# Kernel optimization log

Measured on AMD Instinct MI355X. Metric: run time of the kernel, lower is better.

## Reference

```python
import jax, jax.numpy as jnp
import numpy as np

D_MODEL = 1024
N_HEADS = 16
D_HEAD = D_MODEL // N_HEADS


def setup_inputs() -> dict:
    key = jax.random.key(0)
    ks = jax.random.split(key, 11)
    B, T = 2, 2048
    s = 1.0 / np.sqrt(D_MODEL)
    return {
        "query": jax.random.normal(ks[0], (B, T, D_MODEL), dtype=jnp.float32),
        "key": jax.random.normal(ks[1], (B, T, D_MODEL), dtype=jnp.float32),
        "value": jax.random.normal(ks[2], (B, T, D_MODEL), dtype=jnp.float32),
        "Wq": jax.random.normal(ks[3], (D_MODEL, D_MODEL), dtype=jnp.float32) * s,
        "bq": jnp.zeros((D_MODEL,), dtype=jnp.float32),
        "Wk": jax.random.normal(ks[4], (D_MODEL, D_MODEL), dtype=jnp.float32) * s,
        "bk": jnp.zeros((D_MODEL,), dtype=jnp.float32),
        "Wv": jax.random.normal(ks[5], (D_MODEL, D_MODEL), dtype=jnp.float32) * s,
        "bv": jnp.zeros((D_MODEL,), dtype=jnp.float32),
        "Wh": jax.random.normal(ks[6], (D_MODEL, D_MODEL), dtype=jnp.float32) * s,
        "bh": jnp.zeros((D_MODEL,), dtype=jnp.float32),
    }


def reference(query, key, value, Wq, bq, Wk, bk, Wv, bv, Wh, bh):
    B, T_src, _ = query.shape
    T_dst = key.shape[1]
    # torch nn.Linear: y = x @ W.T + b
    Q = query @ Wq.T + bq          # (B, T_src, D)
    K = key @ Wk.T + bk            # (B, T_dst, D)
    V = value @ Wv.T + bv          # (B, T_dst, D)
    Q = Q.reshape(B, T_src, N_HEADS, D_HEAD).transpose(0, 2, 1, 3)  # (B,H,Ts,dh)
    K = K.reshape(B, T_dst, N_HEADS, D_HEAD).transpose(0, 2, 1, 3)  # (B,H,Td,dh)
    V = V.reshape(B, T_dst, N_HEADS, D_HEAD).transpose(0, 2, 1, 3)  # (B,H,Td,dh)
    dot = jnp.einsum("bhsd,bhtd->bhst", Q, K) / np.sqrt(D_HEAD)     # (B,H,Ts,Td)
    scores = jax.nn.softmax(dot, axis=-1)
    out = jnp.einsum("bhst,bhtd->bhsd", scores, V)  # (B,H,Ts,dh)
    # Faithful to source: reshape WITHOUT transposing heads back (source quirk)
    out = out.reshape(B, T_src, D_MODEL)
    return out @ Wh.T + bh
```

## Files before the change

kernel.cpp:

```cpp
#include <hip/hip_runtime.h>
#include <hip/hip_bf16.h>
#include <stdint.h>

typedef __attribute__((ext_vector_type(8))) short bf16x8;
typedef __attribute__((ext_vector_type(4))) short bf16x4;
typedef __attribute__((ext_vector_type(4))) float f32x4;
typedef __attribute__((ext_vector_type(16))) float f32x16;
typedef __attribute__((ext_vector_type(4))) unsigned int u32x4;
typedef __attribute__((ext_vector_type(2))) __bf16 bf16x2n;

#define DEVI __device__ __forceinline__

DEVI short f2b(float f) {
  union { float f; uint32_t u; } x; x.f = f;
  uint32_t r = x.u + 0x7fffu + ((x.u >> 16) & 1u);
  return (short)(r >> 16);
}

DEVI unsigned packbf(float a, float b) {
  bf16x2n v; v[0] = (__bf16)a; v[1] = (__bf16)b;
  return __builtin_bit_cast(unsigned, v);
}

DEVI float exp2f_(float x) {
#if __has_builtin(__builtin_amdgcn_exp2f)
  return __builtin_amdgcn_exp2f(x);
#else
  return __expf(x * 0.6931471805599453f);
#endif
}

DEVI void plswap(unsigned& a, unsigned& b) {
#if __has_builtin(__builtin_amdgcn_permlane32_swap)
  auto r = __builtin_amdgcn_permlane32_swap(a, b, false, false);
  a = r[0]; b = r[1];
#else
  asm volatile("s_nop 1\n\tv_permlane32_swap_b32 %0, %1\n\ts_nop 1" : "+v"(a), "+v"(b));
#endif
}

DEVI float xmax32(float x) {
  unsigned a = __builtin_bit_cast(unsigned, x), b = a;
  plswap(a, b);
  return fmaxf(__builtin_bit_cast(float, a), __builtin_bit_cast(float, b));
}
DEVI float xsum32(float x) {
  unsigned a = __builtin_bit_cast(unsigned, x), b = a;
  plswap(a, b);
  return __builtin_bit_cast(float, a) + __builtin_bit_cast(float, b);
}

DEVI void async16(const void* gsrc, void* lds) {
  __builtin_amdgcn_global_load_lds((__attribute__((address_space(1))) void*)gsrc,
                                   (__attribute__((address_space(3))) void*)lds,
                                   16, 0, 0);
}

__global__ __launch_bounds__(256) void cvt_all(const float* __restrict__ q,
                                               const float* __restrict__ k,
                                               const float* __restrict__ v,
                                               const float* __restrict__ wq,
                                               const float* __restrict__ wk,
                                               const float* __restrict__ wv,
                                               const float* __restrict__ wh,
                                               short* __restrict__ ws) {
  const size_t MT = 4096ull * 1024ull;
  int bid = blockIdx.x;
  const float* src; short* dst; int idx;
  if (bid < 6144) {
    int r = bid >> 11;
    src = (r == 0) ? q : (r == 1) ? k : v;
    dst = ws + (size_t)r * MT;
    idx = (bid & 2047) * 256 + threadIdx.x;
  } else {
    int r = (bid - 6144) >> 9;
    src = (r == 0) ? wq : (r == 1) ? wk : (r == 2) ? wv : wh;
    dst = ws + 3 * MT + (size_t)r * (1024 * 1024);
    idx = ((bid - 6144) & 511) * 256 + threadIdx.x;
  }
  f32x4 a = ((const f32x4*)src)[2 * idx];
  f32x4 b = ((const f32x4*)src)[2 * idx + 1];
  bf16x8 o;
  o[0]=f2b(a[0]); o[1]=f2b(a[1]); o[2]=f2b(a[2]); o[3]=f2b(a[3]);
  o[4]=f2b(b[0]); o[5]=f2b(b[1]); o[6]=f2b(b[2]); o[7]=f2b(b[3]);
  ((bf16x8*)dst)[idx] = o;
}

__global__ __launch_bounds__(256) void gemm_qkv(const short* __restrict__ A0,
                                                const short* __restrict__ A1,
                                                const short* __restrict__ A2,
                                                const short* __restrict__ W0,
                                                const short* __restrict__ W1,
                                                const short* __restrict__ W2,
                                                const float* __restrict__ b0,
                                                const float* __restrict__ b1,
                                                const float* __restrict__ b2,
                                                short* __restrict__ O0,
                                                short* __restrict__ O1,
                                                short* __restrict__ O2) {
  constexpr int Kd = 1024, Nd = 1024;
  const int z = blockIdx.z;
  const short* A  = (z == 0) ? A0 : (z == 1) ? A1 : A2;
  const short* Bt = (z == 0) ? W0 : (z == 1) ? W1 : W2;
  const float* bias = (z == 0) ? b0 : (z == 1) ? b1 : b2;

  __shared__ __attribute__((aligned(128))) char smem[32768];
  char* As = smem;
  char* Bs = smem + 16384;
  const int tid = threadIdx.x, lane = tid & 63, wave = tid >> 6;
  const int m0 = blockIdx.x * 128, n0 = blockIdx.y * 128;
  const int wr = wave >> 1, wc = wave & 1;

  f32x4 acc[4][4];
#pragma unroll
  for (int i = 0; i < 4; i++)
#pragma unroll
    for (int j = 0; j < 4; j++) acc[i][j] = (f32x4)0.0f;

  for (int k0 = 0; k0 < Kd; k0 += 64) {
#pragma unroll
    for (int it = 0; it < 4; ++it) {
      int ci = it * 256 + tid;
      int r = ci >> 3, c8 = ci & 7;
      int sc = c8 ^ (r & 7);
      async16((const char*)A + ((size_t)(m0 + r) * Kd + k0) * 2 + sc * 16,
              As + it * 4096 + wave * 1024);
      async16((const char*)Bt + ((size_t)(n0 + r) * Kd + k0) * 2 + sc * 16,
              Bs + it * 4096 + wave * 1024);
    }
    __syncthreads();
#pragma unroll
    for (int kk = 0; kk < 2; ++kk) {
      bf16x8 af[4], bf[4];
#pragma unroll
      for (int i = 0; i < 4; i++) {
        int r = wr * 64 + i * 16 + (lane & 15);
        int cb = (kk * 64 + ((lane >> 4) << 4)) ^ ((r & 7) << 4);
        af[i] = *(const bf16x8*)(As + r * 128 + cb);
      }
#pragma unroll
      for (int j = 0; j < 4; j++) {
        int r = wc * 64 + j * 16 + (lane & 15);
        int cb = (kk * 64 + ((lane >> 4) << 4)) ^ ((r & 7) << 4);
        bf[j] = *(const bf16x8*)(Bs + r * 128 + cb);
      }
#pragma unroll
      for (int i = 0; i < 4; i++)
#pragma unroll
        for (int j = 0; j < 4; j++)
          acc[i][j] = __builtin_amdgcn_mfma_f32_16x16x32_bf16(af[i], bf[j], acc[i][j], 0, 0, 0);
    }
    __syncthreads();
  }

  const float scale = (z == 0) ? 0.18033688011112043f : 1.0f;
#pragma unroll
  for (int i = 0; i < 4; i++) {
    int mbase = m0 + wr * 64 + i * 16 + ((lane >> 4) << 2);
#pragma unroll
    for (int j = 0; j < 4; j++) {
      int n = n0 + wc * 64 + j * 16 + (lane & 15);
      float bvf = bias[n];
      if (z < 2) {
        short* out = (z == 0) ? O0 : O1;
#pragma unroll
        for (int r = 0; r < 4; r++)
          out[(size_t)(mbase + r) * Nd + n] = f2b((acc[i][j][r] + bvf) * scale);
      } else {
        int b = mbase >> 11, t = mbase & 2047;
        bf16x4 pk;
#pragma unroll
        for (int r = 0; r < 4; r++) pk[r] = f2b(acc[i][j][r] + bvf);
        *(bf16x4*)(O2 + ((size_t)(b * 1024 + n)) * 2048 + t) = pk;
      }
    }
  }
}

__global__ __launch_bounds__(256) void gemm_out(const short* __restrict__ A,
                                                const short* __restrict__ Bt,
                                                const float* __restrict__ bias,
                                                float* __restrict__ out) {
  constexpr int Kd = 1024, Nd = 1024;
  __shared__ __attribute__((aligned(128))) char smem[32768];
  char* As = smem;
  char* Bs = smem + 16384;
  const int tid = threadIdx.x, lane = tid & 63, wave = tid >> 6;
  const int m0 = blockIdx.x * 128, n0 = blockIdx.y * 128;
  const int wr = wave >> 1, wc = wave & 1;

  f32x4 acc[4][4];
#pragma unroll
  for (int i = 0; i < 4; i++)
#pragma unroll
    for (int j = 0; j < 4; j++) acc[i][j] = (f32x4)0.0f;

  for (int k0 = 0; k0 < Kd; k0 += 64) {
#pragma unroll
    for (int it = 0; it < 4; ++it) {
      int ci = it * 256 + tid;
      int r = ci >> 3, c8 = ci & 7;
      int sc = c8 ^ (r & 7);
      async16((const char*)A + ((size_t)(m0 + r) * Kd + k0) * 2 + sc * 16,
              As + it * 4096 + wave * 1024);
      async16((const char*)Bt + ((size_t)(n0 + r) * Kd + k0) * 2 + sc * 16,
              Bs + it * 4096 + wave * 1024);
    }
    __syncthreads();
#pragma unroll
    for (int kk = 0; kk < 2; ++kk) {
      bf16x8 af[4], bf[4];
#pragma unroll
      for (int i = 0; i < 4; i++) {
        int r = wr * 64 + i * 16 + (lane & 15);
        int cb = (kk * 64 + ((lane >> 4) << 4)) ^ ((r & 7) << 4);
        af[i] = *(const bf16x8*)(As + r * 128 + cb);
      }
#pragma unroll
      for (int j = 0; j < 4; j++) {
        int r = wc * 64 + j * 16 + (lane & 15);
        int cb = (kk * 64 + ((lane >> 4) << 4)) ^ ((r & 7) << 4);
        bf[j] = *(const bf16x8*)(Bs + r * 128 + cb);
      }
#pragma unroll
      for (int i = 0; i < 4; i++)
#pragma unroll
        for (int j = 0; j < 4; j++)
          acc[i][j] = __builtin_amdgcn_mfma_f32_16x16x32_bf16(af[i], bf[j], acc[i][j], 0, 0, 0);
    }
    __syncthreads();
  }

#pragma unroll
  for (int i = 0; i < 4; i++) {
    int mbase = m0 + wr * 64 + i * 16 + ((lane >> 4) << 2);
#pragma unroll
    for (int j = 0; j < 4; j++) {
      int n = n0 + wc * 64 + j * 16 + (lane & 15);
      float bvf = bias[n];
#pragma unroll
      for (int r = 0; r < 4; r++)
        out[(size_t)(mbase + r) * Nd + n] = acc[i][j][r] + bvf;
    }
  }
}

__global__ __launch_bounds__(128) void attn_kernel(const short* __restrict__ Q,
                                                   const short* __restrict__ K,
                                                   const short* __restrict__ Vt,
                                                   short* __restrict__ X) {
  constexpr int T = 2048, D = 1024;
  __shared__ __attribute__((aligned(128))) char smem[32768];
  const int tid = threadIdx.x, lane = tid & 63, wave = tid >> 6;
  const int hi1 = lane >> 5, l31 = lane & 31;

  int bid0 = blockIdx.x;
  int bid = (bid0 & 7) * 128 + (bid0 >> 3);
  const int bh = bid >> 5, qt = bid & 31;
  const int b = bh >> 4, h = bh & 15;
  const int qrow = qt * 64 + wave * 32 + l31;

  bf16x8 qf[4];
  {
    const short* qptr = Q + ((size_t)(b * T + qrow)) * D + h * 64 + hi1 * 8;
#pragma unroll
    for (int kk = 0; kk < 4; kk++) qf[kk] = *(const bf16x8*)(qptr + kk * 16);
  }

  f32x16 o0 = (f32x16)0.0f, o1 = (f32x16)0.0f;
  f32x16 lvec = (f32x16)0.0f;
  float m_run = 0.0f;

  const int swz = (l31 & 7) << 4;
  const int rK0 = l31 * 128, rK1 = (32 + l31) * 128;

  auto STAGE = [&](int bufi, int t0) {
    char* Kd = smem + bufi * 8192;
    char* Vd = smem + 16384 + bufi * 8192;
#pragma unroll
    for (int it = 0; it < 4; ++it) {
      int ci = it * 128 + tid;
      int r = ci >> 3, c8 = ci & 7;
      int sc = (c8 ^ (r & 7)) * 16;
      async16((const char*)(K + ((size_t)(b * T + t0 + r)) * D + h * 64) + sc,
              Kd + it * 2048 + wave * 1024);
      async16((const char*)(Vt + ((size_t)(b * 1024 + h * 64 + r)) * T + t0) + sc,
              Vd + it * 2048 + wave * 1024);
    }
  };

  STAGE(0, 0);

  for (int it = 0; it < 32; ++it) {
    const int cur = it & 1;
    __syncthreads();
    if (it < 31) STAGE(cur ^ 1, (it + 1) * 64);

    char* Kb = smem + cur * 8192;
    char* Vb = smem + 16384 + cur * 8192;

    f32x16 s0 = (f32x16)(-m_run), s1 = (f32x16)(-m_run);
    __builtin_amdgcn_s_setprio(1);
#pragma unroll
    for (int kk = 0; kk < 4; kk++) {
      int cb = (kk * 32 + hi1 * 16) ^ swz;
      bf16x8 ak0 = *(const bf16x8*)(Kb + rK0 + cb);
      s0 = __builtin_amdgcn_mfma_f32_32x32x16_bf16(ak0, qf[kk], s0, 0, 0, 0);
      bf16x8 ak1 = *(const bf16x8*)(Kb + rK1 + cb);
      s1 = __builtin_amdgcn_mfma_f32_32x32x16_bf16(ak1, qf[kk], s1, 0, 0, 0);
    }
    __builtin_amdgcn_s_setprio(0);

    if (it == 0) {
      float t8[8];
#pragma unroll
      for (int i = 0; i < 8; i++)
        t8[i] = fmaxf(fmaxf(s0[i], s0[i + 8]), fmaxf(s1[i], s1[i + 8]));
      float ta = fmaxf(fmaxf(t8[0], t8[1]), t8[2]);
      float tb = fmaxf(fmaxf(t8[3], t8[4]), t8[5]);
      float tm = fmaxf(fmaxf(t8[6], t8[7]), fmaxf(ta, tb));
      m_run = xmax32(tm);
#pragma unroll
      for (int i = 0; i < 16; i++) { s0[i] -= m_run; s1[i] -= m_run; }
    }

#pragma unroll
    for (int i = 0; i < 16; i++) {
      s0[i] = exp2f_(s0[i]);
      s1[i] = exp2f_(s1[i]);
    }
    lvec += s0;
    lvec += s1;

    unsigned w[16];
#pragma unroll
    for (int r2 = 0; r2 < 4; r2++)
#pragma unroll
      for (int wi = 0; wi < 2; wi++) {
        w[r2 * 2 + wi]     = packbf(s0[r2 * 4 + 2 * wi], s0[r2 * 4 + 2 * wi + 1]);
        w[8 + r2 * 2 + wi] = packbf(s1[r2 * 4 + 2 * wi], s1[r2 * 4 + 2 * wi + 1]);
      }
    bf16x8 ap[4];
#pragma unroll
    for (int kk = 0; kk < 4; kk++) {
      u32x4 t4;
#pragma unroll
      for (int wi = 0; wi < 2; wi++) {
        unsigned a = w[(kk >> 1) * 8 + (kk & 1) * 4 + wi];
        unsigned c = w[(kk >> 1) * 8 + (kk & 1) * 4 + 2 + wi];
        plswap(a, c);
        t4[wi] = a; t4[2 + wi] = c;
      }
      ap[kk] = __builtin_bit_cast(bf16x8, t4);
    }

    __builtin_amdgcn_s_setprio(1);
#pragma unroll
    for (int kk = 0; kk < 4; kk++) {
      int cb = (kk * 32 + hi1 * 16) ^ swz;
      bf16x8 av0 = *(const bf16x8*)(Vb + rK0 + cb);
      o0 = __builtin_amdgcn_mfma_f32_32x32x16_bf16(av0, ap[kk], o0, 0, 0, 0);
      bf16x8 av1 = *(const bf16x8*)(Vb + rK1 + cb);
      o1 = __builtin_amdgcn_mfma_f32_32x32x16_bf16(av1, ap[kk], o1, 0, 0, 0);
    }
    __builtin_amdgcn_s_setprio(0);
  }

  float l0 = (lvec[0] + lvec[1]) + (lvec[2] + lvec[3]);
  float l1 = (lvec[4] + lvec[5]) + (lvec[6] + lvec[7]);
  float l2 = (lvec[8] + lvec[9]) + (lvec[10] + lvec[11]);
  float l3 = (lvec[12] + lvec[13]) + (lvec[14] + lvec[15]);
  float l_run = xsum32((l0 + l1) + (l2 + l3));
  float inv = 1.0f / l_run;

  size_t xoff = ((size_t)(b * T + h * 128 + (qrow >> 4))) * D + ((qrow & 15) << 6) + hi1 * 4;
#pragma unroll
  for (int ntd = 0; ntd < 2; ntd++) {
#pragma unroll
    for (int rg = 0; rg < 4; rg++) {
      bf16x4 pk;
#pragma unroll
      for (int j = 0; j < 4; j++) {
        float v = (ntd == 0) ? o0[rg * 4 + j] : o1[rg * 4 + j];
        pk[j] = f2b(v * inv);
      }
      *(bf16x4*)(X + xoff + ntd * 32 + rg * 8) = pk;
    }
  }
}

extern "C" void kernel_launch(void* const* d_in, const int* in_sizes, int n_in,
                              void* d_out, int out_size, void* d_ws, size_t ws_size,
                              hipStream_t stream) {
  (void)in_sizes; (void)n_in; (void)out_size; (void)ws_size;
  const float* query = (const float*)d_in[0];
  const float* key   = (const float*)d_in[1];
  const float* value = (const float*)d_in[2];
  const float* Wq = (const float*)d_in[3];
  const float* bq = (const float*)d_in[4];
  const float* Wk = (const float*)d_in[5];
  const float* bk = (const float*)d_in[6];
  const float* Wv = (const float*)d_in[7];
  const float* bv = (const float*)d_in[8];
  const float* Wh = (const float*)d_in[9];
  const float* bh = (const float*)d_in[10];

  short* ws = (short*)d_ws;
  const size_t MT = 4096ull * 1024ull;
  short* qin_b = ws;
  short* kin_b = ws + MT;
  short* vin_b = ws + 2 * MT;
  short* Wq_b  = ws + 3 * MT;
  short* Wk_b  = Wq_b + 1024 * 1024;
  short* Wv_b  = Wk_b + 1024 * 1024;
  short* Wh_b  = Wv_b + 1024 * 1024;
  short* Qb    = ws + 4 * MT;
  short* Kb    = ws + 5 * MT;
  short* Vtb   = ws + 6 * MT;
  short* Xb    = ws + 7 * MT;

  cvt_all<<<8192, 256, 0, stream>>>(query, key, value, Wq, Wk, Wv, Wh, ws);

  gemm_qkv<<<dim3(32, 8, 3), 256, 0, stream>>>(qin_b, kin_b, vin_b,
                                               Wq_b, Wk_b, Wv_b,
                                               bq, bk, bv,
                                               Qb, Kb, Vtb);

  attn_kernel<<<1024, 128, 0, stream>>>(Qb, Kb, Vtb, Xb);

  gemm_out<<<dim3(32, 8), 256, 0, stream>>>(Xb, Wh_b, bh, (float*)d_out);
}
```

Measured before the change: 132.4 us.

## Fuse fp32-to-bf16 activation conversion into QKV GEMM A-tile loads

Activation inputs are no longer converted to bf16 by a separate pass. The QKV GEMM now reads fp32 query/key/value directly, converts them in registers and writes swizzled bf16 into LDS. Only the weights still go through a smaller conversion kernel. This removes a full write and re-read of three 4096x1024 activation tensors. In exchange each GEMM block reads twice the bytes for A, and the A loads become synchronous register loads instead of async global-to-LDS copies, which can expose latency. Because N is tiled into 8 column blocks, each A row is now re-read as fp32 by all 8 of them.

```diff
diff --git a/kernel.cpp b/kernel.cpp
--- a/kernel.cpp
+++ b/kernel.cpp
@@ -56,28 +56,16 @@
                                    16, 0, 0);
 }
 
-__global__ __launch_bounds__(256) void cvt_all(const float* __restrict__ q,
-                                               const float* __restrict__ k,
-                                               const float* __restrict__ v,
-                                               const float* __restrict__ wq,
-                                               const float* __restrict__ wk,
-                                               const float* __restrict__ wv,
-                                               const float* __restrict__ wh,
-                                               short* __restrict__ ws) {
-  const size_t MT = 4096ull * 1024ull;
+__global__ __launch_bounds__(256) void cvt_w(const float* __restrict__ wq,
+                                             const float* __restrict__ wk,
+                                             const float* __restrict__ wv,
+                                             const float* __restrict__ wh,
+                                             short* __restrict__ dstbase) {
   int bid = blockIdx.x;
-  const float* src; short* dst; int idx;
-  if (bid < 6144) {
-    int r = bid >> 11;
-    src = (r == 0) ? q : (r == 1) ? k : v;
-    dst = ws + (size_t)r * MT;
-    idx = (bid & 2047) * 256 + threadIdx.x;
-  } else {
-    int r = (bid - 6144) >> 9;
-    src = (r == 0) ? wq : (r == 1) ? wk : (r == 2) ? wv : wh;
-    dst = ws + 3 * MT + (size_t)r * (1024 * 1024);
-    idx = ((bid - 6144) & 511) * 256 + threadIdx.x;
-  }
+  int r = bid >> 9;
+  const float* src = (r == 0) ? wq : (r == 1) ? wk : (r == 2) ? wv : wh;
+  short* dst = dstbase + (size_t)r * (1024 * 1024);
+  int idx = (bid & 511) * 256 + threadIdx.x;
   f32x4 a = ((const f32x4*)src)[2 * idx];
   f32x4 b = ((const f32x4*)src)[2 * idx + 1];
   bf16x8 o;
@@ -86,9 +74,9 @@
   ((bf16x8*)dst)[idx] = o;
 }
 
-__global__ __launch_bounds__(256) void gemm_qkv(const short* __restrict__ A0,
-                                                const short* __restrict__ A1,
-                                                const short* __restrict__ A2,
+__global__ __launch_bounds__(256) void gemm_qkv(const float* __restrict__ A0f,
+                                                const float* __restrict__ A1f,
+                                                const float* __restrict__ A2f,
                                                 const short* __restrict__ W0,
                                                 const short* __restrict__ W1,
                                                 const short* __restrict__ W2,
@@ -100,7 +88,7 @@
                                                 short* __restrict__ O2) {
   constexpr int Kd = 1024, Nd = 1024;
   const int z = blockIdx.z;
-  const short* A  = (z == 0) ? A0 : (z == 1) ? A1 : A2;
+  const float* Af = (z == 0) ? A0f : (z == 1) ? A1f : A2f;
   const short* Bt = (z == 0) ? W0 : (z == 1) ? W1 : W2;
   const float* bias = (z == 0) ? b0 : (z == 1) ? b1 : b2;
 
@@ -111,6 +99,10 @@
   const int m0 = blockIdx.x * 128, n0 = blockIdx.y * 128;
   const int wr = wave >> 1, wc = wave & 1;
 
+  const int ar = tid >> 1, ahalf = tid & 1;
+  const int arsw = ar & 7;
+  const float* abase = Af + (size_t)(m0 + ar) * Kd + ahalf * 32;
+
   f32x4 acc[4][4];
 #pragma unroll
   for (int i = 0; i < 4; i++)
@@ -123,10 +115,20 @@
       int ci = it * 256 + tid;
       int r = ci >> 3, c8 = ci & 7;
       int sc = c8 ^ (r & 7);
-      async16((const char*)A + ((size_t)(m0 + r) * Kd + k0) * 2 + sc * 16,
-              As + it * 4096 + wave * 1024);
       async16((const char*)Bt + ((size_t)(n0 + r) * Kd + k0) * 2 + sc * 16,
               Bs + it * 4096 + wave * 1024);
+    }
+    {
+      const f32x4* ap = (const f32x4*)(abase + k0);
+#pragma unroll
+      for (int j = 0; j < 4; ++j) {
+        f32x4 u = ap[2 * j];
+        f32x4 v = ap[2 * j + 1];
+        u32x4 pk;
+        pk[0] = packbf(u[0], u[1]); pk[1] = packbf(u[2], u[3]);
+        pk[2] = packbf(v[0], v[1]); pk[3] = packbf(v[2], v[3]);
+        *(u32x4*)(As + ar * 128 + (((ahalf * 4 + j) ^ arsw) << 4)) = pk;
+      }
     }
     __syncthreads();
 #pragma unroll
@@ -407,21 +409,18 @@
 
   short* ws = (short*)d_ws;
   const size_t MT = 4096ull * 1024ull;
-  short* qin_b = ws;
-  short* kin_b = ws + MT;
-  short* vin_b = ws + 2 * MT;
-  short* Wq_b  = ws + 3 * MT;
-  short* Wk_b  = Wq_b + 1024 * 1024;
-  short* Wv_b  = Wk_b + 1024 * 1024;
-  short* Wh_b  = Wv_b + 1024 * 1024;
-  short* Qb    = ws + 4 * MT;
-  short* Kb    = ws + 5 * MT;
-  short* Vtb   = ws + 6 * MT;
-  short* Xb    = ws + 7 * MT;
-
-  cvt_all<<<8192, 256, 0, stream>>>(query, key, value, Wq, Wk, Wv, Wh, ws);
-
-  gemm_qkv<<<dim3(32, 8, 3), 256, 0, stream>>>(qin_b, kin_b, vin_b,
+  short* Wq_b = ws;
+  short* Wk_b = Wq_b + 1024 * 1024;
+  short* Wv_b = Wk_b + 1024 * 1024;
+  short* Wh_b = Wv_b + 1024 * 1024;
+  short* Qb   = ws + 4 * 1024 * 1024;
+  short* Kb   = Qb + MT;
+  short* Vtb  = Kb + MT;
+  short* Xb   = Vtb + MT;
+
+  cvt_w<<<2048, 256, 0, stream>>>(Wq, Wk, Wv, Wh, ws);
+
+  gemm_qkv<<<dim3(32, 8, 3), 256, 0, stream>>>(query, key, value,
                                                Wq_b, Wk_b, Wv_b,
                                                bq, bk, bv,
                                                Qb, Kb, Vtb);
```

Measured after the change: 156.2 us. 1.18x slower.
